# Kernel optimization log

Measured on AMD Instinct MI355X. Metric: run time of the kernel, lower is better.

The kernel has to match this reference:

```python
import jax, jax.numpy as jnp
import numpy as np

HIDDEN = 1024
BATCH = 32
SEQ = 2048


def setup_inputs() -> dict:
    key = jax.random.key(0)
    ks = jax.random.split(key, 7)
    s = 1.0 / np.sqrt(HIDDEN)  # torch Linear default init range
    x = jax.random.normal(ks[0], (BATCH, SEQ, HIDDEN), dtype=jnp.float32)
    Wq = jax.random.uniform(ks[1], (HIDDEN, HIDDEN), jnp.float32, -s, s)
    bq = jax.random.uniform(ks[2], (HIDDEN,), jnp.float32, -s, s)
    Wk = jax.random.uniform(ks[3], (HIDDEN, HIDDEN), jnp.float32, -s, s)
    bk = jax.random.uniform(ks[4], (HIDDEN,), jnp.float32, -s, s)
    Wv = jax.random.uniform(ks[5], (HIDDEN, HIDDEN), jnp.float32, -s, s)
    bv = jax.random.uniform(ks[6], (HIDDEN,), jnp.float32, -s, s)
    return {"x": x, "Wq": Wq, "bq": bq, "Wk": Wk, "bk": bk, "Wv": Wv, "bv": bv}


def reference(x, Wq, bq, Wk, bk, Wv, bv):
    # x: (B, S, H). torch Linear: y = x @ W.T + b
    scale = jnp.sqrt(jnp.asarray(x.shape[-1], x.dtype))
    # Only the last row of the score matrix is used -> only last query needed.
    q_last = x[:, -1, :] @ Wq.T + bq               # (B, H)
    K = jnp.einsum('bsh,dh->bsd', x, Wk) + bk      # (B, S, H)
    V = jnp.einsum('bsh,dh->bsd', x, Wv) + bv      # (B, S, H)
    scores = jnp.einsum('bd,bsd->bs', q_last, K) / scale  # (B, S)
    weights = jax.nn.softmax(scores, axis=-1)      # (B, S)
    context = jnp.einsum('bs,bsd->bd', weights, V) # (B, H)
    return context, weights
```

## Files before the change

### kernel.cpp

```cpp
#include <hip/hip_runtime.h>

#define HIDDEN 1024
#define BATCH 32
#define SEQ 2048
#define NCHUNK 16
#define CHUNK 128

__device__ __forceinline__ float wave_sum(float v) {
#pragma unroll
    for (int off = 32; off > 0; off >>= 1) v += __shfl_xor(v, off, 64);
    return v;
}

__device__ __forceinline__ float dot4(float4 a, float4 b) {
    return a.x * b.x + a.y * b.y + a.z * b.z + a.w * b.w;
}

__global__ __launch_bounds__(256) void k_matvec(const float* __restrict__ W,
                                                const float* __restrict__ vin,
                                                size_t vstride,
                                                const float* __restrict__ bias,
                                                float* __restrict__ y) {
    int wave = blockIdx.x * 4 + (threadIdx.x >> 6);
    int lane = threadIdx.x & 63;
    int b = wave >> 10;
    int d = wave & 1023;
    const float* vr = vin + (size_t)b * vstride;
    const float* wr = W + ((size_t)d << 10);
    float acc = 0.f;
#pragma unroll
    for (int j = 0; j < 4; ++j)
        acc += dot4(*(const float4*)(vr + j * 256 + lane * 4),
                    *(const float4*)(wr + j * 256 + lane * 4));
    acc = wave_sum(acc);
    if (lane == 0) y[wave] = acc + bias[d];
}

__global__ __launch_bounds__(64) void k_c(const float* __restrict__ q,
                                          const float* __restrict__ bk,
                                          float* __restrict__ c) {
    int b = blockIdx.x;
    int lane = threadIdx.x;
    const float* qr = q + (b << 10);
    float acc = 0.f;
#pragma unroll
    for (int j = 0; j < 4; ++j)
        acc += dot4(*(const float4*)(qr + j * 256 + lane * 4),
                    *(const float4*)(bk + j * 256 + lane * 4));
    acc = wave_sum(acc);
    if (lane == 0) c[b] = acc * (1.0f / 32.0f);
}

__global__ __launch_bounds__(256) void k_qk(const float* __restrict__ Wk,
                                            const float* __restrict__ q,
                                            float* __restrict__ qk) {
    int b = blockIdx.x >> 2;
    int h = ((blockIdx.x & 3) << 8) | threadIdx.x;
    const float* qr = q + (b << 10);
    float acc = 0.f;
#pragma unroll 8
    for (int d = 0; d < HIDDEN; ++d)
        acc = fmaf(Wk[((size_t)d << 10) | h], qr[d], acc);
    qk[(b << 10) | h] = acc * (1.0f / 32.0f);
}

__global__ __launch_bounds__(256) void k_attn(const float* __restrict__ x,
                                              const float* __restrict__ qk,
                                              const float* __restrict__ cb,
                                              float* __restrict__ scores,
                                              float* __restrict__ bacc,
                                              float* __restrict__ bml) {
    int blk = blockIdx.x;
    int b = blk >> 4;
    int s0 = (blk & 15) * CHUNK;
    int wid = threadIdx.x >> 6, lane = threadIdx.x & 63;

    const float* qkr = qk + (b << 10);
    float4 qv[4];
#pragma unroll
    for (int j = 0; j < 4; ++j) qv[j] = *(const float4*)(qkr + j * 256 + lane * 4);
    float cbv = cb[b];

    float m = -1e30f, l = 0.f;
    float4 acc[4];
#pragma unroll
    for (int j = 0; j < 4; ++j) acc[j] = make_float4(0.f, 0.f, 0.f, 0.f);

    for (int i = 0; i < CHUNK / 4; ++i) {
        int s = s0 + (i << 2) + wid;
        const float* xr = x + ((size_t)b * SEQ + s) * HIDDEN;
        float4 xv[4];
#pragma unroll
        for (int j = 0; j < 4; ++j) xv[j] = *(const float4*)(xr + j * 256 + lane * 4);
        float dt = 0.f;
#pragma unroll
        for (int j = 0; j < 4; ++j) dt += dot4(xv[j], qv[j]);
        float sc = wave_sum(dt) + cbv;
        if (lane == 0) scores[b * SEQ + s] = sc;
        float mn = fmaxf(m, sc);
        float f = __expf(m - mn);
        float p = __expf(sc - mn);
        l = l * f + p;
#pragma unroll
        for (int j = 0; j < 4; ++j) {
            acc[j].x = acc[j].x * f + p * xv[j].x;
            acc[j].y = acc[j].y * f + p * xv[j].y;
            acc[j].z = acc[j].z * f + p * xv[j].z;
            acc[j].w = acc[j].w * f + p * xv[j].w;
        }
        m = mn;
    }

    __shared__ float sacc[4][HIDDEN];
    __shared__ float sm[4], sl[4];
#pragma unroll
    for (int j = 0; j < 4; ++j)
        *(float4*)&sacc[wid][j * 256 + lane * 4] = acc[j];
    if (lane == 0) { sm[wid] = m; sl[wid] = l; }
    __syncthreads();
    float M = fmaxf(fmaxf(sm[0], sm[1]), fmaxf(sm[2], sm[3]));
    float f0 = __expf(sm[0] - M), f1 = __expf(sm[1] - M);
    float f2 = __expf(sm[2] - M), f3 = __expf(sm[3] - M);
    float L = sl[0] * f0 + sl[1] * f1 + sl[2] * f2 + sl[3] * f3;
    int h = threadIdx.x << 2;
    float4 a0 = *(const float4*)&sacc[0][h];
    float4 a1 = *(const float4*)&sacc[1][h];
    float4 a2 = *(const float4*)&sacc[2][h];
    float4 a3 = *(const float4*)&sacc[3][h];
    float4 r;
    r.x = a0.x * f0 + a1.x * f1 + a2.x * f2 + a3.x * f3;
    r.y = a0.y * f0 + a1.y * f1 + a2.y * f2 + a3.y * f3;
    r.z = a0.z * f0 + a1.z * f1 + a2.z * f2 + a3.z * f3;
    r.w = a0.w * f0 + a1.w * f1 + a2.w * f2 + a3.w * f3;
    *(float4*)&bacc[((size_t)blk << 10) + h] = r;
    if (threadIdx.x == 0) { bml[blk * 2] = M; bml[blk * 2 + 1] = L; }
}

__global__ __launch_bounds__(256) void k_finalize(const float* __restrict__ bacc,
                                                  const float* __restrict__ bml,
                                                  float* __restrict__ weights,
                                                  float* __restrict__ xb) {
    int b = blockIdx.x;
    float M = -1e30f;
#pragma unroll
    for (int i = 0; i < NCHUNK; ++i) M = fmaxf(M, bml[(b * NCHUNK + i) * 2]);
    float fs[NCHUNK];
    float L = 0.f;
#pragma unroll
    for (int i = 0; i < NCHUNK; ++i) {
        fs[i] = __expf(bml[(b * NCHUNK + i) * 2] - M);
        L += fs[i] * bml[(b * NCHUNK + i) * 2 + 1];
    }
    float invL = 1.f / L;
    int h = threadIdx.x << 2;
    float4 r = make_float4(0.f, 0.f, 0.f, 0.f);
#pragma unroll
    for (int i = 0; i < NCHUNK; ++i) {
        float4 a = *(const float4*)&bacc[((size_t)(b * NCHUNK + i) << 10) + h];
        float f = fs[i] * invL;
        r.x += f * a.x; r.y += f * a.y; r.z += f * a.z; r.w += f * a.w;
    }
    *(float4*)&xb[(b << 10) + h] = r;
#pragma unroll
    for (int i = 0; i < SEQ / 256; ++i) {
        int s = threadIdx.x + i * 256;
        float sc = weights[b * SEQ + s];
        weights[b * SEQ + s] = __expf(sc - M) * invL;
    }
}

extern "C" void kernel_launch(void* const* d_in, const int* in_sizes, int n_in,
                              void* d_out, int out_size, void* d_ws, size_t ws_size,
                              hipStream_t stream) {
    const float* x  = (const float*)d_in[0];
    const float* Wq = (const float*)d_in[1];
    const float* bq = (const float*)d_in[2];
    const float* Wk = (const float*)d_in[3];
    const float* bk = (const float*)d_in[4];
    const float* Wv = (const float*)d_in[5];
    const float* bv = (const float*)d_in[6];

    float* out = (float*)d_out;
    float* ctx = out;
    float* wts = out + BATCH * HIDDEN;

    float* ws   = (float*)d_ws;
    float* q    = ws;
    float* qk   = q + BATCH * HIDDEN;
    float* cb   = qk + BATCH * HIDDEN;
    float* xb   = cb + 64;
    float* bml  = xb + BATCH * HIDDEN;
    float* bacc = bml + 2 * BATCH * NCHUNK;

    k_matvec<<<dim3((BATCH * HIDDEN) / 4), dim3(256), 0, stream>>>(
        Wq, x + (size_t)(SEQ - 1) * HIDDEN, (size_t)SEQ * HIDDEN, bq, q);
    k_c<<<dim3(BATCH), dim3(64), 0, stream>>>(q, bk, cb);
    k_qk<<<dim3(BATCH * 4), dim3(256), 0, stream>>>(Wk, q, qk);
    k_attn<<<dim3(BATCH * NCHUNK), dim3(256), 0, stream>>>(x, qk, cb, wts, bacc, bml);
    k_finalize<<<dim3(BATCH), dim3(256), 0, stream>>>(bacc, bml, wts, xb);
    k_matvec<<<dim3((BATCH * HIDDEN) / 4), dim3(256), 0, stream>>>(
        Wv, xb, (size_t)HIDDEN, bv, ctx);
}
```

Measured before the change: 463.4 us.

## Split qk reduction across waves, shrink attention chunks, double-buffer x loads

k_qk now runs 1024 threads per block, splitting the 1024-long reduction over d into four slices that are combined through shared memory. This gives more parallelism to what was a long serial loop over only 128 blocks. k_attn now uses 64 chunks of 32 rows instead of 16 chunks of 128, so there are more blocks to fill the GPU, and it double-buffers the next x row in registers to overlap loads with compute. The finalize step must then combine 4x more partials, and its chunk weights move into shared memory.

Result: faster. 428.4 us (-7.6%).

```diff
diff --git a/kernel.cpp b/kernel.cpp
--- a/kernel.cpp
+++ b/kernel.cpp
@@ -3,8 +3,8 @@
 #define HIDDEN 1024
 #define BATCH 32
 #define SEQ 2048
-#define NCHUNK 16
-#define CHUNK 128
+#define NCHUNK 64
+#define CHUNK 32
 
 __device__ __forceinline__ float wave_sum(float v) {
 #pragma unroll
@@ -51,17 +51,29 @@
     if (lane == 0) c[b] = acc * (1.0f / 32.0f);
 }
 
-__global__ __launch_bounds__(256) void k_qk(const float* __restrict__ Wk,
-                                            const float* __restrict__ q,
-                                            float* __restrict__ qk) {
+__global__ __launch_bounds__(1024) void k_qk(const float* __restrict__ Wk,
+                                             const float* __restrict__ q,
+                                             float* __restrict__ qk) {
     int b = blockIdx.x >> 2;
-    int h = ((blockIdx.x & 3) << 8) | threadIdx.x;
-    const float* qr = q + (b << 10);
-    float acc = 0.f;
-#pragma unroll 8
-    for (int d = 0; d < HIDDEN; ++d)
-        acc = fmaf(Wk[((size_t)d << 10) | h], qr[d], acc);
-    qk[(b << 10) | h] = acc * (1.0f / 32.0f);
+    int hlo = threadIdx.x & 255;
+    int h = ((blockIdx.x & 3) << 8) | hlo;
+    int dc = threadIdx.x >> 8;
+    const float* qr = q + (b << 10) + (dc << 8);
+    const float* wp = Wk + (((size_t)dc << 8) << 10) + h;
+    float a0 = 0.f, a1 = 0.f;
+#pragma unroll 4
+    for (int d = 0; d < 256; d += 2) {
+        a0 = fmaf(wp[(size_t)d << 10], qr[d], a0);
+        a1 = fmaf(wp[(size_t)(d + 1) << 10], qr[d + 1], a1);
+    }
+    __shared__ float red[4][256];
+    red[dc][hlo] = a0 + a1;
+    __syncthreads();
+    if (threadIdx.x < 256) {
+        float s = red[0][threadIdx.x] + red[1][threadIdx.x] +
+                  red[2][threadIdx.x] + red[3][threadIdx.x];
+        qk[(b << 10) | h] = s * (1.0f / 32.0f);
+    }
 }
 
 __global__ __launch_bounds__(256) void k_attn(const float* __restrict__ x,
@@ -71,8 +83,8 @@
                                               float* __restrict__ bacc,
                                               float* __restrict__ bml) {
     int blk = blockIdx.x;
-    int b = blk >> 4;
-    int s0 = (blk & 15) * CHUNK;
+    int b = blk >> 6;
+    int s0 = (blk & 63) * CHUNK;
     int wid = threadIdx.x >> 6, lane = threadIdx.x & 63;
 
     const float* qkr = qk + (b << 10);
@@ -86,30 +98,45 @@
 #pragma unroll
     for (int j = 0; j < 4; ++j) acc[j] = make_float4(0.f, 0.f, 0.f, 0.f);
 
-    for (int i = 0; i < CHUNK / 4; ++i) {
-        int s = s0 + (i << 2) + wid;
-        const float* xr = x + ((size_t)b * SEQ + s) * HIDDEN;
-        float4 xv[4];
-#pragma unroll
-        for (int j = 0; j < 4; ++j) xv[j] = *(const float4*)(xr + j * 256 + lane * 4);
+    const float* xr = x + ((size_t)b * SEQ + s0 + wid) * HIDDEN + lane * 4;
+
+    float4 bufA[4], bufB[4];
+#pragma unroll
+    for (int j = 0; j < 4; ++j) bufA[j] = *(const float4*)(xr + j * 256);
+
+    auto step = [&](float4 (&cur)[4], float4 (&nxt)[4], int i) {
+        if (i < 7) {
+            const float* xn = xr + (size_t)(i + 1) * 4 * HIDDEN;
+#pragma unroll
+            for (int j = 0; j < 4; ++j) nxt[j] = *(const float4*)(xn + j * 256);
+        }
         float dt = 0.f;
 #pragma unroll
-        for (int j = 0; j < 4; ++j) dt += dot4(xv[j], qv[j]);
+        for (int j = 0; j < 4; ++j) dt += dot4(cur[j], qv[j]);
         float sc = wave_sum(dt) + cbv;
-        if (lane == 0) scores[b * SEQ + s] = sc;
+        if (lane == 0) scores[b * SEQ + s0 + wid + 4 * i] = sc;
         float mn = fmaxf(m, sc);
         float f = __expf(m - mn);
         float p = __expf(sc - mn);
         l = l * f + p;
 #pragma unroll
         for (int j = 0; j < 4; ++j) {
-            acc[j].x = acc[j].x * f + p * xv[j].x;
-            acc[j].y = acc[j].y * f + p * xv[j].y;
-            acc[j].z = acc[j].z * f + p * xv[j].z;
-            acc[j].w = acc[j].w * f + p * xv[j].w;
+            acc[j].x = fmaf(p, cur[j].x, acc[j].x * f);
+            acc[j].y = fmaf(p, cur[j].y, acc[j].y * f);
+            acc[j].z = fmaf(p, cur[j].z, acc[j].z * f);
+            acc[j].w = fmaf(p, cur[j].w, acc[j].w * f);
         }
         m = mn;
-    }
+    };
+
+    step(bufA, bufB, 0);
+    step(bufB, bufA, 1);
+    step(bufA, bufB, 2);
+    step(bufB, bufA, 3);
+    step(bufA, bufB, 4);
+    step(bufB, bufA, 5);
+    step(bufA, bufB, 6);
+    step(bufB, bufA, 7);
 
     __shared__ float sacc[4][HIDDEN];
     __shared__ float sm[4], sl[4];
@@ -144,21 +171,24 @@
     float M = -1e30f;
 #pragma unroll
     for (int i = 0; i < NCHUNK; ++i) M = fmaxf(M, bml[(b * NCHUNK + i) * 2]);
-    float fs[NCHUNK];
     float L = 0.f;
+    __shared__ float fs[NCHUNK];
 #pragma unroll
     for (int i = 0; i < NCHUNK; ++i) {
-        fs[i] = __expf(bml[(b * NCHUNK + i) * 2] - M);
-        L += fs[i] * bml[(b * NCHUNK + i) * 2 + 1];
+        float f = __expf(bml[(b * NCHUNK + i) * 2] - M);
+        L += f * bml[(b * NCHUNK + i) * 2 + 1];
+        if (threadIdx.x == 0) fs[i] = f;
     }
     float invL = 1.f / L;
+    __syncthreads();
     int h = threadIdx.x << 2;
     float4 r = make_float4(0.f, 0.f, 0.f, 0.f);
 #pragma unroll
     for (int i = 0; i < NCHUNK; ++i) {
         float4 a = *(const float4*)&bacc[((size_t)(b * NCHUNK + i) << 10) + h];
         float f = fs[i] * invL;
-        r.x += f * a.x; r.y += f * a.y; r.z += f * a.z; r.w += f * a.w;
+        r.x = fmaf(f, a.x, r.x); r.y = fmaf(f, a.y, r.y);
+        r.z = fmaf(f, a.z, r.z); r.w = fmaf(f, a.w, r.w);
     }
     *(float4*)&xb[(b << 10) + h] = r;
 #pragma unroll
@@ -195,7 +225,7 @@
     k_matvec<<<dim3((BATCH * HIDDEN) / 4), dim3(256), 0, stream>>>(
         Wq, x + (size_t)(SEQ - 1) * HIDDEN, (size_t)SEQ * HIDDEN, bq, q);
     k_c<<<dim3(BATCH), dim3(64), 0, stream>>>(q, bk, cb);
-    k_qk<<<dim3(BATCH * 4), dim3(256), 0, stream>>>(Wk, q, qk);
+    k_qk<<<dim3(BATCH * 4), dim3(1024), 0, stream>>>(Wk, q, qk);
     k_attn<<<dim3(BATCH * NCHUNK), dim3(256), 0, stream>>>(x, qk, cb, wts, bacc, bml);
     k_finalize<<<dim3(BATCH), dim3(256), 0, stream>>>(bacc, bml, wts, xb);
     k_matvec<<<dim3((BATCH * HIDDEN) / 4), dim3(256), 0, stream>>>(
```
